# Kernel tuning notes

Measured on AMD Instinct MI355X. Metric: run time of the kernel, lower is better.

## Reference

```python
import jax, jax.numpy as jnp
import numpy as np

DIM_HEAD = 128
HEADS = 16
SCALE = DIM_HEAD ** -0.5


def rotate_half(t):
    # '... (j d) -> ... j d' with j=2: split into first/second halves
    x1, x2 = jnp.split(t, 2, axis=-1)
    return jnp.concatenate((-x2, x1), axis=-1)


def apply_rope(pos, t):
    # pos: [n, d]; t: [..., n, d]
    return t * jnp.cos(pos) + rotate_half(t) * jnp.sin(pos)


def setup_inputs() -> dict:
    key = jax.random.key(0)
    k0, k1, k2, k3 = jax.random.split(key, 4)
    b, n, dim = 2, 2048, 2048
    inner = HEADS * DIM_HEAD
    return {
        "x": jax.random.normal(k0, (b, n, dim), jnp.float32),
        "Wq": jax.random.normal(k1, (dim, inner), jnp.float32) * 0.02,
        "Wkv": jax.random.normal(k2, (dim, 2 * DIM_HEAD), jnp.float32) * 0.02,
        "Wout": jax.random.normal(k3, (inner, dim), jnp.float32) * 0.02,
    }


def reference(x, Wq, Wkv, Wout):
    b, n, dim = x.shape
    # projections from the UN-normalized x (norm in original is dead code)
    q = x @ Wq                               # [b, n, h*d]
    kv = x @ Wkv                             # [b, n, 2d]
    k, v = jnp.split(kv, 2, axis=-1)         # each [b, n, d] (multi-query)
    q = q.reshape(b, n, HEADS, DIM_HEAD).transpose(0, 2, 1, 3)  # [b,h,n,d]

    # rotary positions
    inv_freq = 1.0 / (10000.0 ** (jnp.arange(0, DIM_HEAD, 2, dtype=jnp.float32) / DIM_HEAD))
    freqs = jnp.arange(n, dtype=jnp.float32)[:, None] * inv_freq[None, :]
    pos = jnp.concatenate((freqs, freqs), axis=-1)  # [n, d]

    q = apply_rope(pos, q) * SCALE
    k = apply_rope(pos, k)

    sim = jnp.einsum('bhid,bjd->bhij', q, k)  # [b,h,n,n]
    causal_mask = jnp.triu(jnp.ones((n, n), dtype=bool), 1)
    neg = -jnp.finfo(sim.dtype).max
    sim = jnp.where(causal_mask, neg, sim)
    sim = sim - jax.lax.stop_gradient(jnp.max(sim, axis=-1, keepdims=True))
    attn = jax.nn.softmax(sim, axis=-1)

    out = jnp.einsum('bhij,bjd->bhid', attn, v)          # [b,h,n,d]
    out = out.transpose(0, 2, 1, 3).reshape(b, n, HEADS * DIM_HEAD)
    return out @ Wout
```

## Files before the change

### kernel.cpp

```cpp
#include <hip/hip_runtime.h>
#include <hip/hip_bf16.h>
#include <cstddef>
#include <cstdint>

#define BATCH 2
#define SEQ   2048
#define DIM   2048
#define HEADS 16
#define DHEAD 128
#define INNER (HEADS * DHEAD)
#define MROWS (BATCH * SEQ)
#define ATT_SCALE 0.08838834764831845f
#define QK_SCALE (0.08838834764831845f * 1.4426950408889634f)
#define NEG_LOG2_10000_DIV64 (-13.287712379549449f / 64.0f)
#define M_HAT 12.0f

typedef __attribute__((ext_vector_type(8))) short short8;
typedef __attribute__((ext_vector_type(4))) short short4v;
typedef __attribute__((ext_vector_type(4))) float f32x4;

static __device__ __forceinline__ short f2bf(float x) {
    uint32_t u = __float_as_uint(x);
    uint32_t r = (u + 0x7fffu + ((u >> 16) & 1u)) >> 16;
    return (short)r;
}
static __device__ __forceinline__ float bf2f(short s) {
    return __uint_as_float(((uint32_t)(uint16_t)s) << 16);
}
static __device__ __forceinline__ short2 f2bf2(float a, float b) {
    __hip_bfloat162 h = __float22bfloat162_rn(make_float2(a, b));
    return *reinterpret_cast<short2*>(&h);
}

static __device__ __forceinline__ void glds16(const short* g, short* l) {
    __builtin_amdgcn_global_load_lds(
        (const __attribute__((address_space(1))) unsigned int*)g,
        (__attribute__((address_space(3))) unsigned int*)l, 16, 0, 0);
}

static __device__ __forceinline__ int swz_row(int r) {
    return (r & 3) | ((r >> 1) & 4);
}

static __device__ __forceinline__ void tcast_body(const float* __restrict__ W,
                                                  short* __restrict__ Wt,
                                                  int R, int C, int bx, int by,
                                                  int tid, float (*tile)[65]) {
    const int c0 = bx * 64, r0 = by * 64;
#pragma unroll
    for (int t = 0; t < 16; ++t) {
        int idx = tid + t * 256;
        int row = idx >> 6, col = idx & 63;
        tile[row][col] = W[(size_t)(r0 + row) * C + c0 + col];
    }
    __syncthreads();
#pragma unroll
    for (int t = 0; t < 16; ++t) {
        int idx = tid + t * 256;
        int r = idx >> 6, c = idx & 63;
        Wt[(size_t)(c0 + r) * R + r0 + c] = f2bf(tile[c][r]);
    }
}

__global__ __launch_bounds__(256) void prep(const float* __restrict__ x,
                                            short* __restrict__ xb,
                                            const float* __restrict__ Wq,
                                            short* __restrict__ Wt,
                                            const float* __restrict__ Wkv,
                                            short* __restrict__ Wkvt,
                                            const float* __restrict__ Wout,
                                            short* __restrict__ WtO,
                                            float2* __restrict__ lut) {
    __shared__ float tile[64][65];
    const int bid = blockIdx.x;
    const int tid = threadIdx.x;
    if (bid < 8192) {
        int i = bid * 256 + tid;
        float4 v = ((const float4*)x)[i];
        short2 s01 = f2bf2(v.x, v.y), s23 = f2bf2(v.z, v.w);
        short4v s = {s01.x, s01.y, s23.x, s23.y};
        ((short4v*)xb)[i] = s;
    } else if (bid < 9216) {
        int t = bid - 8192;
        tcast_body(Wq, Wt, DIM, INNER, t & 31, t >> 5, tid, tile);
    } else if (bid < 9344) {
        int t = bid - 9216;
        tcast_body(Wkv, Wkvt, DIM, 256, t & 3, t >> 2, tid, tile);
    } else if (bid < 10368) {
        int t = bid - 9344;
        tcast_body(Wout, WtO, INNER, DIM, t & 31, t >> 5, tid, tile);
    } else {
        int t = (bid - 10368) * 256 + tid;
        int pos = t >> 6, j = t & 63;
        float ang = (float)pos * exp2f((float)j * NEG_LOG2_10000_DIV64);
        lut[t] = make_float2(cosf(ang), sinf(ang));
    }
}

__global__ __launch_bounds__(256) void gemm_qkv(const short* __restrict__ A,
                                                const short* __restrict__ Bt,
                                                short* __restrict__ qout,
                                                short* __restrict__ kvout) {
    __shared__ __align__(16) short sA[128 * 32];
    __shared__ __align__(16) short sB[128 * 32];
    const int K = DIM;

    const int tid = threadIdx.x;
    const int w = tid >> 6, lane = tid & 63;
    const int ln = lane & 15, qr = lane >> 4;
    const int bm = blockIdx.y * 128, bn = blockIdx.x * 128;
    const int wm = (w >> 1) * 64, wn = (w & 1) * 64;

    const f32x4 zero4 = {0.f, 0.f, 0.f, 0.f};
    f32x4 acc[4][4];
#pragma unroll
    for (int mt = 0; mt < 4; ++mt)
#pragma unroll
        for (int nt = 0; nt < 4; ++nt) acc[mt][nt] = zero4;

    const int srow = lane >> 2;
    const short* pA = A + (size_t)(bm + w * 32 + srow) * K + (lane & 3) * 8;
    const short* pB = Bt + (size_t)(bn + w * 32 + srow) * K + (lane & 3) * 8;
    short* lA = &sA[(w * 32) * 32];
    short* lB = &sB[(w * 32) * 32];

    for (int k0 = 0; k0 < K; k0 += 32) {
        __syncthreads();
        glds16(pA + k0, lA);
        glds16(pA + k0 + (size_t)16 * K, lA + 512);
        glds16(pB + k0, lB);
        glds16(pB + k0 + (size_t)16 * K, lB + 512);
        __syncthreads();

        short8 af[4], bfr[4];
#pragma unroll
        for (int mt = 0; mt < 4; ++mt)
            af[mt] = *(const short8*)&sA[(wm + mt * 16 + ln) * 32 + qr * 8];
#pragma unroll
        for (int nt = 0; nt < 4; ++nt)
            bfr[nt] = *(const short8*)&sB[(wn + nt * 16 + ln) * 32 + qr * 8];
#pragma unroll
        for (int mt = 0; mt < 4; ++mt)
#pragma unroll
            for (int nt = 0; nt < 4; ++nt)
                acc[mt][nt] = __builtin_amdgcn_mfma_f32_16x16x32_bf16(
                    af[mt], bfr[nt], acc[mt][nt], 0, 0, 0);
    }

    short* C;
    int stride, colb;
    if (bn < INNER) { C = qout; stride = INNER; colb = bn; }
    else            { C = kvout; stride = 256;  colb = bn - INNER; }
#pragma unroll
    for (int mt = 0; mt < 4; ++mt)
#pragma unroll
        for (int nt = 0; nt < 4; ++nt)
#pragma unroll
            for (int r = 0; r < 4; ++r)
                C[(size_t)(bm + wm + mt * 16 + qr * 4 + r) * stride +
                  colb + wn + nt * 16 + ln] = f2bf(acc[mt][nt][r]);
}

__global__ __launch_bounds__(256) void gemm_bt(const short* __restrict__ A,
                                               const short* __restrict__ Bt,
                                               float* __restrict__ C,
                                               int M, int N, int K) {
    __shared__ __align__(16) short sA[128 * 32];
    __shared__ __align__(16) short sB[128 * 32];

    const int tid = threadIdx.x;
    const int w = tid >> 6, lane = tid & 63;
    const int ln = lane & 15, qr = lane >> 4;
    const int bm = blockIdx.y * 128, bn = blockIdx.x * 128;
    const int wm = (w >> 1) * 64, wn = (w & 1) * 64;

    const f32x4 zero4 = {0.f, 0.f, 0.f, 0.f};
    f32x4 acc[4][4];
#pragma unroll
    for (int mt = 0; mt < 4; ++mt)
#pragma unroll
        for (int nt = 0; nt < 4; ++nt) acc[mt][nt] = zero4;

    const int srow = lane >> 2;
    const short* pA = A + (size_t)(bm + w * 32 + srow) * K + (lane & 3) * 8;
    const short* pB = Bt + (size_t)(bn + w * 32 + srow) * K + (lane & 3) * 8;
    short* lA = &sA[(w * 32) * 32];
    short* lB = &sB[(w * 32) * 32];

    for (int k0 = 0; k0 < K; k0 += 32) {
        __syncthreads();
        glds16(pA + k0, lA);
        glds16(pA + k0 + (size_t)16 * K, lA + 512);
        glds16(pB + k0, lB);
        glds16(pB + k0 + (size_t)16 * K, lB + 512);
        __syncthreads();

        short8 af[4], bfr[4];
#pragma unroll
        for (int mt = 0; mt < 4; ++mt)
            af[mt] = *(const short8*)&sA[(wm + mt * 16 + ln) * 32 + qr * 8];
#pragma unroll
        for (int nt = 0; nt < 4; ++nt)
            bfr[nt] = *(const short8*)&sB[(wn + nt * 16 + ln) * 32 + qr * 8];
#pragma unroll
        for (int mt = 0; mt < 4; ++mt)
#pragma unroll
            for (int nt = 0; nt < 4; ++nt)
                acc[mt][nt] = __builtin_amdgcn_mfma_f32_16x16x32_bf16(
                    af[mt], bfr[nt], acc[mt][nt], 0, 0, 0);
    }

#pragma unroll
    for (int mt = 0; mt < 4; ++mt)
#pragma unroll
        for (int nt = 0; nt < 4; ++nt)
#pragma unroll
            for (int r = 0; r < 4; ++r)
                C[(size_t)(bm + wm + mt * 16 + qr * 4 + r) * N +
                  bn + wn + nt * 16 + ln] = acc[mt][nt][r];
}

__global__ __launch_bounds__(256) void rope_q_v(short* __restrict__ qb,
                                                const float2* __restrict__ lut) {
    int idx = blockIdx.x * 256 + threadIdx.x;
    int c = idx & 7;
    int rh = idx >> 3;
    int pos = (rh >> 4) & (SEQ - 1);
    short* row = qb + ((size_t)rh << 7);
    short8 a8 = *(short8*)&row[c * 8];
    short8 b8 = *(short8*)&row[64 + c * 8];
    const float2* lp = &lut[pos * 64 + c * 8];
    short8 o1, o2;
#pragma unroll
    for (int e = 0; e < 8; e += 2) {
        float2 cs0 = lp[e], cs1 = lp[e + 1];
        float a0 = bf2f(a8[e]), b0 = bf2f(b8[e]);
        float a1 = bf2f(a8[e + 1]), b1 = bf2f(b8[e + 1]);
        short2 p1 = f2bf2((a0 * cs0.x - b0 * cs0.y) * QK_SCALE,
                          (a1 * cs1.x - b1 * cs1.y) * QK_SCALE);
        short2 p2 = f2bf2((b0 * cs0.x + a0 * cs0.y) * QK_SCALE,
                          (b1 * cs1.x + a1 * cs1.y) * QK_SCALE);
        o1[e] = p1.x; o1[e + 1] = p1.y;
        o2[e] = p2.x; o2[e + 1] = p2.y;
    }
    *(short8*)&row[c * 8] = o1;
    *(short8*)&row[64 + c * 8] = o2;
}

__global__ __launch_bounds__(256) void prep_kv(const short* __restrict__ kvbb,
                                               short* __restrict__ kb,
                                               short* __restrict__ vt,
                                               const float2* __restrict__ lut) {
    __shared__ float tile[64][65];
    const int bid = blockIdx.x;
    const int tid = threadIdx.x;
    if (bid < 128) {
        const int b = bid >> 6;
        const int tile_id = bid & 63;
        const int p0 = (tile_id >> 1) * 64;
        const int d0 = (tile_id & 1) * 64;
#pragma unroll
        for (int t = 0; t < 16; ++t) {
            int idx = tid + t * 256;
            int row = idx >> 6, col = idx & 63;
            tile[row][col] = bf2f(kvbb[((size_t)(b * SEQ) + p0 + row) * 256 + 128 + d0 + col]);
        }
        __syncthreads();
#pragma unroll
        for (int t = 0; t < 16; ++t) {
            int idx = tid + t * 256;
            int r = idx >> 6, c = idx & 63;
            vt[((size_t)(b * DHEAD) + d0 + r) * SEQ + p0 + c] = f2bf(tile[c][r]);
        }
    } else {
        int t = (bid - 128) * 256 + tid;
        int c = t & 7;
        int bn = t >> 3;
        int pos = bn & (SEQ - 1);
        const short* row = kvbb + (size_t)bn * 256;
        short* orow = kb + ((size_t)bn << 7);
        short8 a8 = *(const short8*)&row[c * 8];
        short8 b8 = *(const short8*)&row[64 + c * 8];
        const float2* lp = &lut[pos * 64 + c * 8];
        short8 o1, o2;
#pragma unroll
        for (int e = 0; e < 8; e += 2) {
            float2 cs0 = lp[e], cs1 = lp[e + 1];
            float a0 = bf2f(a8[e]), b0 = bf2f(b8[e]);
            float a1 = bf2f(a8[e + 1]), b1 = bf2f(b8[e + 1]);
            short2 p1 = f2bf2(a0 * cs0.x - b0 * cs0.y, a1 * cs1.x - b1 * cs1.y);
            short2 p2 = f2bf2(b0 * cs0.x + a0 * cs0.y, b1 * cs1.x + a1 * cs1.y);
            o1[e] = p1.x; o1[e + 1] = p1.y;
            o2[e] = p2.x; o2[e + 1] = p2.y;
        }
        *(short8*)&orow[c * 8] = o1;
        *(short8*)&orow[64 + c * 8] = o2;
    }
}

__global__ __launch_bounds__(512) void attn_mfma(const short* __restrict__ qb,
                                                 const short* __restrict__ kb,
                                                 const short* __restrict__ vt,
                                                 short* __restrict__ o) {
    __shared__ __align__(16) short sK[2][2][64 * 128];
    __shared__ __align__(16) short sV[2][2][128 * 64];
    __shared__ float lred[4][2][64];

    const int bid = blockIdx.x;
    const int p = bid & 7;
    const int bh = bid >> 3;
    const int h = bh & (HEADS - 1);
    const int b = bh >> 4;

    const int tid = threadIdx.x;
    const int w = tid >> 6;
    const int g = w >> 2;
    const int wg = w & 3;
    const int lane = tid & 63;
    const int ln = lane & 15;
    const int qr = lane >> 4;

    const short* kbase = kb + (size_t)b * SEQ * DHEAD;
    const short* vbase = vt + (size_t)b * DHEAD * SEQ;

    int offK[4], offV[4], ldsK[4], ldsV[4];
#pragma unroll
    for (int t = 0; t < 4; ++t) {
        int rk = wg * 16 + t * 4 + (lane >> 4);
        int ck = (lane & 15) ^ swz_row(rk);
        offK[t] = rk * DHEAD + ck * 8;
        ldsK[t] = (wg * 16 + t * 4) * 128;
        int rv = wg * 32 + t * 8 + (lane >> 3);
        int cv = (lane & 7) ^ swz_row(rv);
        offV[t] = rv * SEQ + cv * 8;
        ldsV[t] = (wg * 32 + t * 8) * 64;
    }

    for (int ph = 0; ph < 2; ++ph) {
        const int it = ph ? p : (15 - p);
        const int i0 = it * 128;
        const int njt = 2 * it + 2;
        const int half = njt >> 1;

        short8 qf[2][4];
#pragma unroll
        for (int qs = 0; qs < 2; ++qs) {
            const size_t qrow =
                ((size_t)(b * SEQ + i0 + wg * 32 + qs * 16 + ln)) * INNER + h * DHEAD;
#pragma unroll
            for (int ks = 0; ks < 4; ++ks)
                qf[qs][ks] = *(const short8*)&qb[qrow + ks * 32 + qr * 8];
        }

        const f32x4 zero4 = {0.f, 0.f, 0.f, 0.f};
        f32x4 oa[2][8];
#pragma unroll
        for (int qs = 0; qs < 2; ++qs)
#pragma unroll
            for (int dt = 0; dt < 8; ++dt) oa[qs][dt] = zero4;
        float lsum[2] = {0.f, 0.f};

        __syncthreads();
        {
            const size_t kof = (size_t)g * 64 * DHEAD;
            const size_t vof = (size_t)g * 64;
#pragma unroll
            for (int t = 0; t < 4; ++t)
                glds16(kbase + kof + offK[t], &sK[g][0][ldsK[t]]);
#pragma unroll
            for (int t = 0; t < 4; ++t)
                glds16(vbase + vof + offV[t], &sV[g][0][ldsV[t]]);
        }

        for (int k = 0; k < half; ++k) {
            const int cur = k & 1;
            const int jt = 2 * k + g;
            __syncthreads();
            if (k + 1 < half) {
                const size_t kof = (size_t)(jt + 2) * 64 * DHEAD;
                const size_t vof = (size_t)(jt + 2) * 64;
#pragma unroll
                for (int t = 0; t < 4; ++t)
                    glds16(kbase + kof + offK[t], &sK[g][cur ^ 1][ldsK[t]]);
#pragma unroll
                for (int t = 0; t < 4; ++t)
                    glds16(vbase + vof + offV[t], &sV[g][cur ^ 1][ldsV[t]]);
            }

            f32x4 sacc[2][4];
#pragma unroll
            for (int qs = 0; qs < 2; ++qs)
#pragma unroll
                for (int nt = 0; nt < 4; ++nt) sacc[qs][nt] = zero4;
#pragma unroll
            for (int nt = 0; nt < 4; ++nt) {
                const int row = ((nt >> 1) << 5) + ((ln >> 2) << 3) +
                                ((nt & 1) << 2) + (ln & 3);
                const int sw = ln & 7;
#pragma unroll
                for (int ks = 0; ks < 4; ++ks) {
                    short8 kf = *(const short8*)&sK[g][cur][row * 128 + ((4 * ks + qr) ^ sw) * 8];
                    sacc[0][nt] = __builtin_amdgcn_mfma_f32_16x16x32_bf16(
                        kf, qf[0][ks], sacc[0][nt], 0, 0, 0);
                    sacc[1][nt] = __builtin_amdgcn_mfma_f32_16x16x32_bf16(
                        kf, qf[1][ks], sacc[1][nt], 0, 0, 0);
                }
            }

            short8 pb[2][2];
#pragma unroll
            for (int qs = 0; qs < 2; ++qs) {
                const int ig = i0 + wg * 32 + qs * 16 + ln;
                if (jt * 64 + 63 > ig) {
#pragma unroll
                    for (int nt = 0; nt < 4; ++nt)
#pragma unroll
                        for (int r = 0; r < 4; ++r) {
                            int jg = jt * 64 + ((nt >> 1) << 5) + qr * 8 +
                                     ((nt & 1) << 2) + r;
                            if (jg > ig) sacc[qs][nt][r] = -3.0e38f;
                        }
                }
                float rs = 0.f;
                float pv[4][4];
#pragma unroll
                for (int nt = 0; nt < 4; ++nt)
#pragma unroll
                    for (int r = 0; r < 4; ++r) {
                        float e = exp2f(sacc[qs][nt][r] - M_HAT);
                        pv[nt][r] = e;
                        rs += e;
                    }
                rs += __shfl_xor(rs, 16);
                rs += __shfl_xor(rs, 32);
                lsum[qs] += rs;
#pragma unroll
                for (int kb2 = 0; kb2 < 2; ++kb2) {
                    short2* pp = (short2*)&pb[qs][kb2];
                    pp[0] = f2bf2(pv[2 * kb2][0], pv[2 * kb2][1]);
                    pp[1] = f2bf2(pv[2 * kb2][2], pv[2 * kb2][3]);
                    pp[2] = f2bf2(pv[2 * kb2 + 1][0], pv[2 * kb2 + 1][1]);
                    pp[3] = f2bf2(pv[2 * kb2 + 1][2], pv[2 * kb2 + 1][3]);
                }
            }

#pragma unroll
            for (int kb2 = 0; kb2 < 2; ++kb2) {
#pragma unroll
                for (int dt = 0; dt < 8; ++dt) {
                    const int row = dt * 16 + ln;
                    short8 vf = *(const short8*)&sV[g][cur][row * 64 +
                        ((4 * kb2 + qr) ^ swz_row(row)) * 8];
                    oa[0][dt] = __builtin_amdgcn_mfma_f32_16x16x32_bf16(
                        vf, pb[0][kb2], oa[0][dt], 0, 0, 0);
                    oa[1][dt] = __builtin_amdgcn_mfma_f32_16x16x32_bf16(
                        vf, pb[1][kb2], oa[1][dt], 0, 0, 0);
                }
            }
        }

        f32x4* cb = (f32x4*)&sK[1][0][0];
        __syncthreads();
        if (g == 1) {
#pragma unroll
            for (int dt = 0; dt < 8; ++dt)
                cb[dt * 256 + wg * 64 + lane] = oa[0][dt];
            lred[wg][0][lane] = lsum[0];
            lred[wg][1][lane] = lsum[1];
        }
        __syncthreads();
        if (g == 0) {
#pragma unroll
            for (int dt = 0; dt < 8; ++dt)
                oa[0][dt] += cb[dt * 256 + wg * 64 + lane];
            lsum[0] += lred[wg][0][lane];
            lsum[1] += lred[wg][1][lane];
        }
        __syncthreads();
        if (g == 1) {
#pragma unroll
            for (int dt = 0; dt < 8; ++dt)
                cb[dt * 256 + wg * 64 + lane] = oa[1][dt];
        }
        __syncthreads();
        if (g == 0) {
#pragma unroll
            for (int dt = 0; dt < 8; ++dt)
                oa[1][dt] += cb[dt * 256 + wg * 64 + lane];
#pragma unroll
            for (int qs = 0; qs < 2; ++qs) {
                const float invl = 1.f / lsum[qs];
                short* orow = o + ((size_t)(b * SEQ + i0 + wg * 32 + qs * 16 + ln)) * INNER +
                              h * DHEAD;
#pragma unroll
                for (int dt = 0; dt < 8; ++dt) {
                    short2 s01 = f2bf2(oa[qs][dt][0] * invl, oa[qs][dt][1] * invl);
                    short2 s23 = f2bf2(oa[qs][dt][2] * invl, oa[qs][dt][3] * invl);
                    short4v sv = {s01.x, s01.y, s23.x, s23.y};
                    *(short4v*)&orow[dt * 16 + qr * 4] = sv;
                }
            }
        }
    }
}

extern "C" void kernel_launch(void* const* d_in, const int* in_sizes, int n_in,
                              void* d_out, int out_size, void* d_ws, size_t ws_size,
                              hipStream_t stream) {
    const float* x    = (const float*)d_in[0];
    const float* Wq   = (const float*)d_in[1];
    const float* Wkv  = (const float*)d_in[2];
    const float* Wout = (const float*)d_in[3];
    float* out = (float*)d_out;

    short* xb    = (short*)d_ws;
    short* Wt    = xb + (size_t)MROWS * DIM;
    short* Wkvt  = Wt + (size_t)DIM * INNER;
    short* WtO   = Wkvt + (size_t)256 * DIM;
    short* qb    = WtO + (size_t)DIM * INNER;
    short* kvbb  = qb + (size_t)MROWS * INNER;
    short* kb    = kvbb + (size_t)MROWS * 256;
    short* vt    = kb + (size_t)MROWS * DHEAD;
    float2* lut  = (float2*)(vt + (size_t)BATCH * DHEAD * SEQ);
    short* ob    = xb;

    prep<<<10880, 256, 0, stream>>>(x, xb, Wq, Wt, Wkv, Wkvt, Wout, WtO, lut);
    gemm_qkv<<<dim3(18, 32), 256, 0, stream>>>(xb, Wt, qb, kvbb);
    rope_q_v<<<(MROWS * HEADS * 8) / 256, 256, 0, stream>>>(qb, lut);
    prep_kv<<<256, 256, 0, stream>>>(kvbb, kb, vt, lut);
    attn_mfma<<<256, 512, 0, stream>>>(qb, kb, vt, ob);
    gemm_bt<<<dim3(DIM / 128, MROWS / 128), 256, 0, stream>>>(ob, WtO, out, MROWS, DIM, INNER);
}
```

Baseline: 288.4 us.

## Restructure attention to one query tile per block without KV split

The attention kernel now launches one block per (query tile, batch-head) pair, ordered longest-first, instead of pairing two query tiles per block. The two wave groups that split the KV range and reduced through shared memory are replaced by eight waves that each own 16 query rows over the full KV range. This removes the cross-group reduction and halves LDS use to allow more resident blocks (launch bounds hint 4). In exchange, the causal load balance now relies on the hardware scheduler, and waves skip fully masked tiles while still taking part in the block barriers.

```diff
diff --git a/kernel.cpp b/kernel.cpp
--- a/kernel.cpp
+++ b/kernel.cpp
@@ -298,24 +298,22 @@
     }
 }
 
-__global__ __launch_bounds__(512) void attn_mfma(const short* __restrict__ qb,
-                                                 const short* __restrict__ kb,
-                                                 const short* __restrict__ vt,
-                                                 short* __restrict__ o) {
-    __shared__ __align__(16) short sK[2][2][64 * 128];
-    __shared__ __align__(16) short sV[2][2][128 * 64];
-    __shared__ float lred[4][2][64];
+__global__ __launch_bounds__(512, 4) void attn_mfma(const short* __restrict__ qb,
+                                                    const short* __restrict__ kb,
+                                                    const short* __restrict__ vt,
+                                                    short* __restrict__ o) {
+    __shared__ __align__(16) short sK[2][64 * 128];
+    __shared__ __align__(16) short sV[2][128 * 64];
 
     const int bid = blockIdx.x;
-    const int p = bid & 7;
-    const int bh = bid >> 3;
+    const int cc = bid >> 5;
+    const int it = (cc < 8) ? (15 - cc) : (cc - 8);
+    const int bh = bid & 31;
     const int h = bh & (HEADS - 1);
     const int b = bh >> 4;
 
     const int tid = threadIdx.x;
     const int w = tid >> 6;
-    const int g = w >> 2;
-    const int wg = w & 3;
     const int lane = tid & 63;
     const int ln = lane & 15;
     const int qr = lane >> 4;
@@ -323,184 +321,128 @@
     const short* kbase = kb + (size_t)b * SEQ * DHEAD;
     const short* vbase = vt + (size_t)b * DHEAD * SEQ;
 
-    int offK[4], offV[4], ldsK[4], ldsV[4];
-#pragma unroll
-    for (int t = 0; t < 4; ++t) {
-        int rk = wg * 16 + t * 4 + (lane >> 4);
+    int offK[2], offV[2], ldsK[2], ldsV[2];
+#pragma unroll
+    for (int t = 0; t < 2; ++t) {
+        int rk = w * 8 + t * 4 + (lane >> 4);
         int ck = (lane & 15) ^ swz_row(rk);
         offK[t] = rk * DHEAD + ck * 8;
-        ldsK[t] = (wg * 16 + t * 4) * 128;
-        int rv = wg * 32 + t * 8 + (lane >> 3);
+        ldsK[t] = (w * 8 + t * 4) * 128;
+        int rv = w * 16 + t * 8 + (lane >> 3);
         int cv = (lane & 7) ^ swz_row(rv);
         offV[t] = rv * SEQ + cv * 8;
-        ldsV[t] = (wg * 32 + t * 8) * 64;
-    }
-
-    for (int ph = 0; ph < 2; ++ph) {
-        const int it = ph ? p : (15 - p);
-        const int i0 = it * 128;
-        const int njt = 2 * it + 2;
-        const int half = njt >> 1;
-
-        short8 qf[2][4];
-#pragma unroll
-        for (int qs = 0; qs < 2; ++qs) {
-            const size_t qrow =
-                ((size_t)(b * SEQ + i0 + wg * 32 + qs * 16 + ln)) * INNER + h * DHEAD;
-#pragma unroll
-            for (int ks = 0; ks < 4; ++ks)
-                qf[qs][ks] = *(const short8*)&qb[qrow + ks * 32 + qr * 8];
-        }
-
-        const f32x4 zero4 = {0.f, 0.f, 0.f, 0.f};
-        f32x4 oa[2][8];
-#pragma unroll
-        for (int qs = 0; qs < 2; ++qs)
-#pragma unroll
-            for (int dt = 0; dt < 8; ++dt) oa[qs][dt] = zero4;
-        float lsum[2] = {0.f, 0.f};
-
-        __syncthreads();
-        {
-            const size_t kof = (size_t)g * 64 * DHEAD;
-            const size_t vof = (size_t)g * 64;
-#pragma unroll
-            for (int t = 0; t < 4; ++t)
-                glds16(kbase + kof + offK[t], &sK[g][0][ldsK[t]]);
-#pragma unroll
-            for (int t = 0; t < 4; ++t)
-                glds16(vbase + vof + offV[t], &sV[g][0][ldsV[t]]);
-        }
-
-        for (int k = 0; k < half; ++k) {
-            const int cur = k & 1;
-            const int jt = 2 * k + g;
-            __syncthreads();
-            if (k + 1 < half) {
-                const size_t kof = (size_t)(jt + 2) * 64 * DHEAD;
-                const size_t vof = (size_t)(jt + 2) * 64;
-#pragma unroll
-                for (int t = 0; t < 4; ++t)
-                    glds16(kbase + kof + offK[t], &sK[g][cur ^ 1][ldsK[t]]);
-#pragma unroll
-                for (int t = 0; t < 4; ++t)
-                    glds16(vbase + vof + offV[t], &sV[g][cur ^ 1][ldsV[t]]);
+        ldsV[t] = (w * 16 + t * 8) * 64;
+    }
+
+    const int i0 = it * 128;
+    const int njt = 2 * it + 2;
+    const int ig = i0 + w * 16 + ln;
+    const int igmax = i0 + w * 16 + 15;
+
+    short8 qf[4];
+    {
+        const size_t qrow = ((size_t)(b * SEQ + i0 + w * 16 + ln)) * INNER + h * DHEAD;
+#pragma unroll
+        for (int ks = 0; ks < 4; ++ks)
+            qf[ks] = *(const short8*)&qb[qrow + ks * 32 + qr * 8];
+    }
+
+    const f32x4 zero4 = {0.f, 0.f, 0.f, 0.f};
+    f32x4 oa[8];
+#pragma unroll
+    for (int dt = 0; dt < 8; ++dt) oa[dt] = zero4;
+    float lsum = 0.f;
+
+#pragma unroll
+    for (int t = 0; t < 2; ++t) glds16(kbase + offK[t], &sK[0][ldsK[t]]);
+#pragma unroll
+    for (int t = 0; t < 2; ++t) glds16(vbase + offV[t], &sV[0][ldsV[t]]);
+
+    for (int jt = 0; jt < njt; ++jt) {
+        const int cur = jt & 1;
+        __syncthreads();
+        if (jt + 1 < njt) {
+            const size_t kof = (size_t)(jt + 1) * 64 * DHEAD;
+            const size_t vof = (size_t)(jt + 1) * 64;
+#pragma unroll
+            for (int t = 0; t < 2; ++t)
+                glds16(kbase + kof + offK[t], &sK[cur ^ 1][ldsK[t]]);
+#pragma unroll
+            for (int t = 0; t < 2; ++t)
+                glds16(vbase + vof + offV[t], &sV[cur ^ 1][ldsV[t]]);
+        }
+        if (jt * 64 > igmax) continue;
+
+        f32x4 sacc[4];
+#pragma unroll
+        for (int nt = 0; nt < 4; ++nt) sacc[nt] = zero4;
+#pragma unroll
+        for (int nt = 0; nt < 4; ++nt) {
+            const int row = ((nt >> 1) << 5) + ((ln >> 2) << 3) +
+                            ((nt & 1) << 2) + (ln & 3);
+            const int sw = ln & 7;
+#pragma unroll
+            for (int ks = 0; ks < 4; ++ks) {
+                short8 kf = *(const short8*)&sK[cur][row * 128 + ((4 * ks + qr) ^ sw) * 8];
+                sacc[nt] = __builtin_amdgcn_mfma_f32_16x16x32_bf16(
+                    kf, qf[ks], sacc[nt], 0, 0, 0);
             }
-
-            f32x4 sacc[2][4];
-#pragma unroll
-            for (int qs = 0; qs < 2; ++qs)
-#pragma unroll
-                for (int nt = 0; nt < 4; ++nt) sacc[qs][nt] = zero4;
-#pragma unroll
-            for (int nt = 0; nt < 4; ++nt) {
-                const int row = ((nt >> 1) << 5) + ((ln >> 2) << 3) +
-                                ((nt & 1) << 2) + (ln & 3);
-                const int sw = ln & 7;
-#pragma unroll
-                for (int ks = 0; ks < 4; ++ks) {
-                    short8 kf = *(const short8*)&sK[g][cur][row * 128 + ((4 * ks + qr) ^ sw) * 8];
-                    sacc[0][nt] = __builtin_amdgcn_mfma_f32_16x16x32_bf16(
-                        kf, qf[0][ks], sacc[0][nt], 0, 0, 0);
-                    sacc[1][nt] = __builtin_amdgcn_mfma_f32_16x16x32_bf16(
-                        kf, qf[1][ks], sacc[1][nt], 0, 0, 0);
+        }
+
+        if (jt * 64 + 63 > ig) {
+#pragma unroll
+            for (int nt = 0; nt < 4; ++nt)
+#pragma unroll
+                for (int r = 0; r < 4; ++r) {
+                    int jg = jt * 64 + ((nt >> 1) << 5) + qr * 8 +
+                             ((nt & 1) << 2) + r;
+                    if (jg > ig) sacc[nt][r] = -3.0e38f;
                 }
+        }
+        float rs = 0.f;
+        float pv[4][4];
+#pragma unroll
+        for (int nt = 0; nt < 4; ++nt)
+#pragma unroll
+            for (int r = 0; r < 4; ++r) {
+                float e = exp2f(sacc[nt][r] - M_HAT);
+                pv[nt][r] = e;
+                rs += e;
             }
-
-            short8 pb[2][2];
-#pragma unroll
-            for (int qs = 0; qs < 2; ++qs) {
-                const int ig = i0 + wg * 32 + qs * 16 + ln;
-                if (jt * 64 + 63 > ig) {
-#pragma unroll
-                    for (int nt = 0; nt < 4; ++nt)
-#pragma unroll
-                        for (int r = 0; r < 4; ++r) {
-                            int jg = jt * 64 + ((nt >> 1) << 5) + qr * 8 +
-                                     ((nt & 1) << 2) + r;
-                            if (jg > ig) sacc[qs][nt][r] = -3.0e38f;
-                        }
-                }
-                float rs = 0.f;
-                float pv[4][4];
-#pragma unroll
-                for (int nt = 0; nt < 4; ++nt)
-#pragma unroll
-                    for (int r = 0; r < 4; ++r) {
-                        float e = exp2f(sacc[qs][nt][r] - M_HAT);
-                        pv[nt][r] = e;
-                        rs += e;
-                    }
-                rs += __shfl_xor(rs, 16);
-                rs += __shfl_xor(rs, 32);
-                lsum[qs] += rs;
-#pragma unroll
-                for (int kb2 = 0; kb2 < 2; ++kb2) {
-                    short2* pp = (short2*)&pb[qs][kb2];
-                    pp[0] = f2bf2(pv[2 * kb2][0], pv[2 * kb2][1]);
-                    pp[1] = f2bf2(pv[2 * kb2][2], pv[2 * kb2][3]);
-                    pp[2] = f2bf2(pv[2 * kb2 + 1][0], pv[2 * kb2 + 1][1]);
-                    pp[3] = f2bf2(pv[2 * kb2 + 1][2], pv[2 * kb2 + 1][3]);
-                }
+        rs += __shfl_xor(rs, 16);
+        rs += __shfl_xor(rs, 32);
+        lsum += rs;
+        short8 pb[2];
+#pragma unroll
+        for (int kb2 = 0; kb2 < 2; ++kb2) {
+            short2* pp = (short2*)&pb[kb2];
+            pp[0] = f2bf2(pv[2 * kb2][0], pv[2 * kb2][1]);
+            pp[1] = f2bf2(pv[2 * kb2][2], pv[2 * kb2][3]);
+            pp[2] = f2bf2(pv[2 * kb2 + 1][0], pv[2 * kb2 + 1][1]);
+            pp[3] = f2bf2(pv[2 * kb2 + 1][2], pv[2 * kb2 + 1][3]);
+        }
+
+#pragma unroll
+        for (int kb2 = 0; kb2 < 2; ++kb2) {
+#pragma unroll
+            for (int dt = 0; dt < 8; ++dt) {
+                const int row = dt * 16 + ln;
+                short8 vf = *(const short8*)&sV[cur][row * 64 +
+                    ((4 * kb2 + qr) ^ swz_row(row)) * 8];
+                oa[dt] = __builtin_amdgcn_mfma_f32_16x16x32_bf16(
+                    vf, pb[kb2], oa[dt], 0, 0, 0);
             }
-
-#pragma unroll
-            for (int kb2 = 0; kb2 < 2; ++kb2) {
-#pragma unroll
-                for (int dt = 0; dt < 8; ++dt) {
-                    const int row = dt * 16 + ln;
-                    short8 vf = *(const short8*)&sV[g][cur][row * 64 +
-                        ((4 * kb2 + qr) ^ swz_row(row)) * 8];
-                    oa[0][dt] = __builtin_amdgcn_mfma_f32_16x16x32_bf16(
-                        vf, pb[0][kb2], oa[0][dt], 0, 0, 0);
-                    oa[1][dt] = __builtin_amdgcn_mfma_f32_16x16x32_bf16(
-                        vf, pb[1][kb2], oa[1][dt], 0, 0, 0);
-                }
-            }
-        }
-
-        f32x4* cb = (f32x4*)&sK[1][0][0];
-        __syncthreads();
-        if (g == 1) {
-#pragma unroll
-            for (int dt = 0; dt < 8; ++dt)
-                cb[dt * 256 + wg * 64 + lane] = oa[0][dt];
-            lred[wg][0][lane] = lsum[0];
-            lred[wg][1][lane] = lsum[1];
-        }
-        __syncthreads();
-        if (g == 0) {
-#pragma unroll
-            for (int dt = 0; dt < 8; ++dt)
-                oa[0][dt] += cb[dt * 256 + wg * 64 + lane];
-            lsum[0] += lred[wg][0][lane];
-            lsum[1] += lred[wg][1][lane];
-        }
-        __syncthreads();
-        if (g == 1) {
-#pragma unroll
-            for (int dt = 0; dt < 8; ++dt)
-                cb[dt * 256 + wg * 64 + lane] = oa[1][dt];
-        }
-        __syncthreads();
-        if (g == 0) {
-#pragma unroll
-            for (int dt = 0; dt < 8; ++dt)
-                oa[1][dt] += cb[dt * 256 + wg * 64 + lane];
-#pragma unroll
-            for (int qs = 0; qs < 2; ++qs) {
-                const float invl = 1.f / lsum[qs];
-                short* orow = o + ((size_t)(b * SEQ + i0 + wg * 32 + qs * 16 + ln)) * INNER +
-                              h * DHEAD;
-#pragma unroll
-                for (int dt = 0; dt < 8; ++dt) {
-                    short2 s01 = f2bf2(oa[qs][dt][0] * invl, oa[qs][dt][1] * invl);
-                    short2 s23 = f2bf2(oa[qs][dt][2] * invl, oa[qs][dt][3] * invl);
-                    short4v sv = {s01.x, s01.y, s23.x, s23.y};
-                    *(short4v*)&orow[dt * 16 + qr * 4] = sv;
-                }
-            }
-        }
+        }
+    }
+
+    const float invl = 1.f / lsum;
+    short* orow = o + ((size_t)(b * SEQ + i0 + w * 16 + ln)) * INNER + h * DHEAD;
+#pragma unroll
+    for (int dt = 0; dt < 8; ++dt) {
+        short2 s01 = f2bf2(oa[dt][0] * invl, oa[dt][1] * invl);
+        short2 s23 = f2bf2(oa[dt][2] * invl, oa[dt][3] * invl);
+        short4v sv = {s01.x, s01.y, s23.x, s23.y};
+        *(short4v*)&orow[dt * 16 + qr * 4] = sv;
     }
 }
 
@@ -528,6 +470,6 @@
     gemm_qkv<<<dim3(18, 32), 256, 0, stream>>>(xb, Wt, qb, kvbb);
     rope_q_v<<<(MROWS * HEADS * 8) / 256, 256, 0, stream>>>(qb, lut);
     prep_kv<<<256, 256, 0, stream>>>(kvbb, kb, vt, lut);
-    attn_mfma<<<256, 512, 0, stream>>>(qb, kb, vt, ob);
+    attn_mfma<<<512, 512, 0, stream>>>(qb, kb, vt, ob);
     gemm_bt<<<dim3(DIM / 128, MROWS / 128), 256, 0, stream>>>(ob, WtO, out, MROWS, DIM, INNER);
 }
```

After: 290.5 us. About the same (+0.7%).
